# Performance work log

Measured on AMD Instinct MI355X. Metric: run time of the kernel, lower is better.

The kernel has to match this reference:

```python
import jax, jax.numpy as jnp
import numpy as np

BITS = 4
MAXQ = (1 << BITS) - 1      # 15
PACK = 32 // BITS           # 8 values per int32 word
GROUP = 128                 # quantization group size along K


def setup_inputs() -> dict:
    key = jax.random.key(0)
    k0, k1, k2, k3 = jax.random.split(key, 4)
    M, K, N = 4096, 4096, 11008
    G = K // GROUP
    x = jax.random.normal(k0, (M, K), dtype=jnp.float32)
    # packed 4-bit weights: full-range random int32 words (each holds 8 nibbles)
    qweight = jax.random.randint(k1, (K // PACK, N), -(2**31), 2**31 - 1, dtype=jnp.int32)
    # packed zero points: (G, N // PACK) int32 words
    qzeros = jax.random.randint(k2, (G, N // PACK), -(2**31), 2**31 - 1, dtype=jnp.int32)
    # group-wise scales (G, N), small positive values as GPTQ produces
    scales = jax.random.uniform(k3, (G, N), dtype=jnp.float32, minval=1e-3, maxval=1e-2)
    # standard GPTQ grouping: consecutive blocks of GROUP rows share a group
    g_idx = (jnp.arange(K) // GROUP).astype(jnp.int32)
    return {"x": x, "qweight": qweight, "scales": scales, "qzeros": qzeros, "g_idx": g_idx}


def _dequant(qweight, scales, qzeros, g_idx):
    """Unpack int32-packed 4-bit weights and dequantize to float. Returns (K, N)."""
    K = g_idx.shape[0]
    N = qweight.shape[1]
    k = jnp.arange(K)
    # nibble k lives in word k//PACK at bit offset (k%PACK)*BITS
    k_shift = ((k % PACK) * BITS).astype(jnp.int32)
    w = (qweight[k // PACK] >> k_shift[:, None]) & MAXQ              # (K, N) int32 in [0, MAXQ]
    n = jnp.arange(N)
    n_shift = ((n % PACK) * BITS).astype(jnp.int32)
    z = ((qzeros[:, n // PACK] >> n_shift[None, :]) & MAXQ) + 1      # (G, N); kernel adds 1
    return (w - z[g_idx]).astype(scales.dtype) * scales[g_idx]       # (K, N) float


def reference(x, qweight, scales, qzeros, g_idx):
    # C = A @ dequant(B), fp32 accumulation as in the Triton kernel
    W = _dequant(qweight, scales, qzeros, g_idx)
    return jnp.matmul(x, W, preferred_element_type=jnp.float32)
```

## Files before the change

kernel.cpp:

```cpp
#include <hip/hip_runtime.h>
#include <hip/hip_bf16.h>
#include <stdint.h>

typedef _Float16 half8 __attribute__((ext_vector_type(8)));
typedef __attribute__((ext_vector_type(8))) short short8;
typedef __attribute__((ext_vector_type(4))) float floatx4;
typedef __attribute__((ext_vector_type(4))) uint32_t uint32x4;

#define GROUP_SZ 128

__device__ __forceinline__ uint32_t cvt_pk_f16(float lo, float hi) {
    uint32_t r;
    asm("v_cvt_pkrtz_f16_f32 %0, %1, %2" : "=v"(r) : "v"(lo), "v"(hi));
    return r;
}
__device__ __forceinline__ uint32_t pk_add_f16(uint32_t a, uint32_t b) {
    uint32_t r;
    asm("v_pk_add_f16 %0, %1, %2" : "=v"(r) : "v"(a), "v"(b));
    return r;
}
__device__ __forceinline__ uint32_t pk_mul_f16(uint32_t a, uint32_t b) {
    uint32_t r;
    asm("v_pk_mul_f16 %0, %1, %2" : "=v"(r) : "v"(a), "v"(b));
    return r;
}

__global__ __launch_bounds__(256)
void convA_kernel(const float* __restrict__ x, uint4* __restrict__ aws, int total8) {
    int idx = blockIdx.x * 256 + threadIdx.x;
    if (idx >= total8) return;
    const float4* xp = reinterpret_cast<const float4*>(x) + (size_t)idx * 2;
    float4 a = xp[0], b = xp[1];
    uint4 o;
    o.x = cvt_pk_f16(a.x, a.y);
    o.y = cvt_pk_f16(a.z, a.w);
    o.z = cvt_pk_f16(b.x, b.y);
    o.w = cvt_pk_f16(b.z, b.w);
    aws[idx] = o;
}

__global__ __launch_bounds__(256)
void deqB_kernel(const int* __restrict__ qw, const float* __restrict__ sc,
                 const int* __restrict__ qz, char* __restrict__ bws, int K, int N) {
    const int n = blockIdx.x * 256 + threadIdx.x;
    const int wk = blockIdx.y;
    if (n >= N) return;
    const uint32_t w = (uint32_t)qw[(size_t)wk * N + n];
    const int g = wk >> 4;
    const float s = sc[(size_t)g * N + n];
    const uint32_t zw = (uint32_t)qz[(size_t)g * (N >> 3) + (n >> 3)];
    const float zf = -(float)(1025u + ((zw >> ((n & 7) * 4)) & 15u));
    const uint32_t c2 = cvt_pk_f16(zf, zf);
    const uint32_t s2 = cvt_pk_f16(s, s);
    uint32_t oo[4];
    #pragma unroll
    for (int i = 0; i < 4; ++i) {
        const uint32_t tt = w >> (8 * i);
        const uint32_t qi = ((tt & 0xFu) | 0x64006400u) | ((tt << 12) & 0xF0000u);
        oo[i] = pk_mul_f16(pk_add_f16(qi, c2), s2);
    }
    uint4 o; o.x = oo[0]; o.y = oo[1]; o.z = oo[2]; o.w = oo[3];
    const int NKT = K >> 6;
    const int nt = n >> 8, h = (n >> 7) & 1, row = n & 127;
    const int kt = wk >> 3, slot = wk & 7;
    size_t off = ((((size_t)nt * NKT + kt) * 2 + h) * 8 + slot) * 2048 + (size_t)row * 16;
    *reinterpret_cast<uint4*>(bws + off) = o;
}

__global__ __launch_bounds__(512, 2)
void gemm8_kernel(const char* __restrict__ Aws, const char* __restrict__ Bws,
                  float* __restrict__ out, int M, int K, int N) {
    __shared__ char smem[131072];

    const int NT = K >> 6;
    const int nbm = M >> 8, nbn = N >> 8;
    const int nwg = nbm * nbn;
    int bid = blockIdx.x;
    int q = nwg >> 3, r = nwg & 7;
    int xcd = bid & 7, lin = bid >> 3;
    int sid = (xcd < r ? xcd * (q + 1) : r * (q + 1) + (xcd - r) * q) + lin;
    const int bm = sid % nbm, bn = sid / nbm;
    const int m0 = bm << 8, n0 = bn << 8;

    const int tid = threadIdx.x;
    const int lane = tid & 63, w = tid >> 6;
    const int wm = w >> 2, wn = w & 3;
    const int fr = lane & 15, hi = lane >> 4;
    const int r8 = lane >> 3, c8 = lane & 7;

    const uint32_t K2 = (uint32_t)K * 2;
    const char* aBase = Aws + (size_t)m0 * K2;
    uint32_t aOff[2][2];
    #pragma unroll
    for (int h = 0; h < 2; ++h)
        #pragma unroll
        for (int i = 0; i < 2; ++i)
            aOff[h][i] = (uint32_t)(h * 128 + w * 16 + i * 8 + r8) * K2
                       + (uint32_t)((c8 ^ r8) * 16);
    const char* bBase = Bws + (size_t)bn * ((size_t)NT * 32768);
    const uint32_t bOff = (uint32_t)w * 2048u + (uint32_t)lane * 16u;

    auto stageA = [&](uint32_t buf, int h, int kt) {
        #pragma unroll
        for (int i = 0; i < 2; ++i) {
            const char* src = aBase + aOff[h][i] + (uint32_t)kt * 128u;
            char* dst = smem + buf * 65536u + (uint32_t)h * 16384u
                             + (uint32_t)w * 2048u + (uint32_t)i * 1024u;
            __builtin_amdgcn_global_load_lds(
                (const __attribute__((address_space(1))) void*)src,
                (__attribute__((address_space(3))) void*)dst, 16, 0, 0);
        }
    };
    auto stageB = [&](uint32_t buf, int h, int kt) {
        #pragma unroll
        for (int i = 0; i < 2; ++i) {
            const char* src = bBase + bOff + (uint32_t)((kt * 2 + h) * 16384 + i * 1024);
            char* dst = smem + buf * 65536u + 32768u + (uint32_t)h * 16384u
                             + (uint32_t)w * 2048u + (uint32_t)i * 1024u;
            __builtin_amdgcn_global_load_lds(
                (const __attribute__((address_space(1))) void*)src,
                (__attribute__((address_space(3))) void*)dst, 16, 0, 0);
        }
    };

    floatx4 acc[8][4];
    const floatx4 fz = {0.f, 0.f, 0.f, 0.f};
    #pragma unroll
    for (int i = 0; i < 8; ++i)
        #pragma unroll
        for (int j = 0; j < 4; ++j) acc[i][j] = fz;
    half8 af_a[4][2], af_b[4][2];
    half8 bf_x[2][2], bf_y[2][2];

#define LOAD_AF(AF, QM) { _Pragma("unroll") for (int fmi = 0; fmi < 4; ++fmi) { \
    _Pragma("unroll") for (int kk = 0; kk < 2; ++kk) { \
        uint32_t row = (uint32_t)(wm * 128 + ((QM) * 4 + fmi) * 16 + fr); \
        uint32_t p = (uint32_t)((kk * 4 + hi) ^ (fr & 7)); \
        uint32x4 u = *reinterpret_cast<const uint32x4*>(As + row * 128u + p * 16u); \
        AF[fmi][kk] = __builtin_bit_cast(half8, u); } } }

#define LOAD_BF(BF, QN) { _Pragma("unroll") for (int fnj = 0; fnj < 2; ++fnj) { \
    _Pragma("unroll") for (int kk = 0; kk < 2; ++kk) { \
        uint32_t nl = (uint32_t)(wn * 64 + ((QN) * 2 + fnj) * 16 + fr); \
        uint32_t off = (nl >> 7) * 16384u + (uint32_t)(kk * 4 + hi) * 2048u + (nl & 127u) * 16u; \
        uint32x4 u = *reinterpret_cast<const uint32x4*>(Bs + off); \
        BF[fnj][kk] = __builtin_bit_cast(half8, u); } } }

#define MM(AF, BF, QM, QN) { _Pragma("unroll") for (int kk = 0; kk < 2; ++kk) \
    _Pragma("unroll") for (int fmi = 0; fmi < 4; ++fmi) \
    _Pragma("unroll") for (int fnj = 0; fnj < 2; ++fnj) \
        acc[(QM) * 4 + fmi][(QN) * 2 + fnj] = __builtin_amdgcn_mfma_f32_16x16x32_f16( \
            AF[fmi][kk], BF[fnj][kk], acc[(QM) * 4 + fmi][(QN) * 2 + fnj], 0, 0, 0); }

    stageA(0, 0, 0); stageA(0, 1, 0); stageB(0, 0, 0); stageB(0, 1, 0);
    if (NT > 1) { stageA(1, 0, 1); stageA(1, 1, 1); }
    asm volatile("s_waitcnt vmcnt(4)" ::: "memory");
    __builtin_amdgcn_s_barrier();

    for (int t = 0; t < NT; ++t) {
        const uint32_t c = (uint32_t)(t & 1), nb = c ^ 1u;
        const char* As = smem + c * 65536u;
        const char* Bs = As + 32768u;
        const bool st1 = (t + 1 < NT);
        const bool st2 = (t + 2 < NT);
        if (st1) stageB(nb, 0, t + 1);
        LOAD_AF(af_a, 0); LOAD_BF(bf_x, 0);
        __builtin_amdgcn_s_barrier();
        __builtin_amdgcn_s_setprio(1); MM(af_a, bf_x, 0, 0); __builtin_amdgcn_s_setprio(0);
        __builtin_amdgcn_s_barrier();
        if (st1) stageB(nb, 1, t + 1);
        LOAD_AF(af_b, 1);
        __builtin_amdgcn_s_barrier();
        __builtin_amdgcn_s_setprio(1); MM(af_b, bf_x, 1, 0); __builtin_amdgcn_s_setprio(0);
        __builtin_amdgcn_s_barrier();
        if (st2) stageA(c, 0, t + 2);
        LOAD_BF(bf_y, 1);
        __builtin_amdgcn_s_barrier();
        __builtin_amdgcn_s_setprio(1); MM(af_a, bf_y, 0, 1); __builtin_amdgcn_s_setprio(0);
        __builtin_amdgcn_s_barrier();
        if (st2) stageA(c, 1, t + 2);
        __builtin_amdgcn_s_barrier();
        __builtin_amdgcn_s_setprio(1); MM(af_b, bf_y, 1, 1); __builtin_amdgcn_s_setprio(0);
        if (st2) {
            asm volatile("s_waitcnt vmcnt(4)" ::: "memory");
        } else if (st1) {
            asm volatile("s_waitcnt vmcnt(0)" ::: "memory");
        }
        if (st1) __builtin_amdgcn_s_barrier();
    }
#undef LOAD_AF
#undef LOAD_BF
#undef MM

    float* op = out + (size_t)(m0 + wm * 128) * N + n0 + wn * 64;
    #pragma unroll
    for (int fm = 0; fm < 8; ++fm)
        #pragma unroll
        for (int fn = 0; fn < 4; ++fn)
            #pragma unroll
            for (int rr = 0; rr < 4; ++rr)
                op[(size_t)(fm * 16 + hi * 4 + rr) * N + fn * 16 + fr] = acc[fm][fn][rr];
}

__device__ __forceinline__ uint32_t cvt_pk_bf16(float lo, float hi) {
    uint32_t r;
    asm("v_cvt_pk_bf16_f32 %0, %1, %2" : "=v"(r) : "v"(lo), "v"(hi));
    return r;
}
__device__ __forceinline__ uint32_t fswz(uint32_t row, uint32_t byte_in_row) {
    return row * 128u + (byte_in_row ^ ((row & 7u) << 4));
}

__global__ __launch_bounds__(256, 2)
void fused128_kernel(const float* __restrict__ x, const int* __restrict__ qweight,
                     const float* __restrict__ scales, const int* __restrict__ qzeros,
                     float* __restrict__ out, int M, int K, int N) {
    __shared__ char smem[32768];
    char* Ald = smem;
    char* Bld = smem + 16384;
    const int nbm = M / 128, nbn = N / 128;
    const int nwg = nbm * nbn;
    int bid = blockIdx.x;
    int q = nwg >> 3, r = nwg & 7;
    int xcd = bid & 7, lin = bid >> 3;
    int sid = (xcd < r ? xcd * (q + 1) : r * (q + 1) + (xcd - r) * q) + lin;
    int bm = sid / nbn, bn = sid % nbn;
    const int m0 = bm * 128, n0 = bn * 128;
    const int t = threadIdx.x;
    const int lane = t & 63, wave = t >> 6;
    const int tm = t >> 4, tk4 = t & 15;
    const int sn = t & 127, kwh = t >> 7;
    const int gn = n0 + sn;
    const int NT = K / 64;
    float4 av[8]; uint32_t qw[4]; float sc; uint32_t zw;
    const float* xp = x + (size_t)(m0 + tm) * K + tk4 * 4;
    const int* qp = qweight + (size_t)(kwh * 4) * N + gn;
    auto load_tile = [&](int ts) {
        const int k0 = ts * 64;
        #pragma unroll
        for (int i = 0; i < 8; ++i)
            av[i] = *reinterpret_cast<const float4*>(xp + (size_t)i * 16 * K + k0);
        const int g = k0 >> 7;
        sc = scales[(size_t)g * N + gn];
        zw = (uint32_t)qzeros[(size_t)g * (N >> 3) + (gn >> 3)];
        const int* qb = qp + (size_t)(k0 >> 3) * N;
        #pragma unroll
        for (int j = 0; j < 4; ++j) qw[j] = (uint32_t)qb[(size_t)j * N];
    };
    const int zsh = (gn & 7) * 4;
    auto write_tile = [&]() {
        #pragma unroll
        for (int i = 0; i < 8; ++i) {
            uint2 p;
            p.x = cvt_pk_bf16(av[i].x, av[i].y);
            p.y = cvt_pk_bf16(av[i].z, av[i].w);
            *reinterpret_cast<uint2*>(Ald + fswz((uint32_t)(i * 16 + tm), (uint32_t)(tk4 * 8))) = p;
        }
        const float z = (float)((zw >> zsh) & 15u) + 1.0f;
        const float nz = -z * sc;
        #pragma unroll
        for (int j = 0; j < 4; ++j) {
            const uint32_t wv = qw[j];
            float f[8];
            #pragma unroll
            for (int e = 0; e < 8; ++e)
                f[e] = fmaf((float)((wv >> (4 * e)) & 15u), sc, nz);
            uint4 p;
            p.x = cvt_pk_bf16(f[0], f[1]); p.y = cvt_pk_bf16(f[2], f[3]);
            p.z = cvt_pk_bf16(f[4], f[5]); p.w = cvt_pk_bf16(f[6], f[7]);
            *reinterpret_cast<uint4*>(Bld + fswz((uint32_t)sn, (uint32_t)((kwh * 4 + j) * 16))) = p;
        }
    };
    floatx4 acc[4][4];
    const floatx4 fz = {0.f, 0.f, 0.f, 0.f};
    #pragma unroll
    for (int i = 0; i < 4; ++i)
        #pragma unroll
        for (int j = 0; j < 4; ++j) acc[i][j] = fz;
    const int wm = (wave >> 1) * 64, wn = (wave & 1) * 64;
    const int fr = lane & 15;
    const int fkb = ((lane >> 4) * 8) * 2;
    auto compute = [&]() {
        #pragma unroll
        for (int kk = 0; kk < 2; ++kk) {
            short8 afv[4], bfv[4];
            #pragma unroll
            for (int i = 0; i < 4; ++i)
                afv[i] = *reinterpret_cast<const short8*>(
                    Ald + fswz((uint32_t)(wm + i * 16 + fr), (uint32_t)(kk * 64 + fkb)));
            #pragma unroll
            for (int i = 0; i < 4; ++i)
                bfv[i] = *reinterpret_cast<const short8*>(
                    Bld + fswz((uint32_t)(wn + i * 16 + fr), (uint32_t)(kk * 64 + fkb)));
            #pragma unroll
            for (int i = 0; i < 4; ++i)
                #pragma unroll
                for (int j = 0; j < 4; ++j)
                    acc[i][j] = __builtin_amdgcn_mfma_f32_16x16x32_bf16(afv[i], bfv[j], acc[i][j], 0, 0, 0);
        }
    };
    load_tile(0);
    write_tile();
    __syncthreads();
    for (int ts = 0; ts < NT; ++ts) {
        if (ts + 1 < NT) load_tile(ts + 1);
        compute();
        __syncthreads();
        if (ts + 1 < NT) write_tile();
        __syncthreads();
    }
    const int fq = lane >> 4;
    float* op = out + (size_t)(m0 + wm) * N + n0 + wn;
    #pragma unroll
    for (int i = 0; i < 4; ++i)
        #pragma unroll
        for (int j = 0; j < 4; ++j)
            #pragma unroll
            for (int rr = 0; rr < 4; ++rr)
                op[(size_t)(i * 16 + fq * 4 + rr) * N + j * 16 + fr] = acc[i][j][rr];
}

extern "C" void kernel_launch(void* const* d_in, const int* in_sizes, int n_in,
                              void* d_out, int out_size, void* d_ws, size_t ws_size,
                              hipStream_t stream) {
    const float* x       = (const float*)d_in[0];
    const int*   qweight = (const int*)d_in[1];
    const float* scales  = (const float*)d_in[2];
    const int*   qzeros  = (const int*)d_in[3];

    const int K = in_sizes[4];
    const int M = in_sizes[0] / K;
    const int G = K / GROUP_SZ;
    const int N = in_sizes[2] / G;
    float* out = (float*)d_out;

    const size_t needA = (size_t)M * K * 2;
    const size_t needB = (size_t)K * (size_t)N * 2;
    const bool ok = (ws_size >= needA + needB) && (M % 256 == 0) && (N % 256 == 0)
                    && (K % 128 == 0) && (N % 8 == 0);
    if (ok) {
        char* aws = (char*)d_ws;
        char* bws = aws + needA;
        const int total8 = M * (K / 8);
        hipLaunchKernelGGL(convA_kernel, dim3((total8 + 255) / 256), dim3(256), 0, stream,
                           x, (uint4*)aws, total8);
        hipLaunchKernelGGL(deqB_kernel, dim3((N + 255) / 256, K / 8), dim3(256), 0, stream,
                           qweight, scales, qzeros, bws, K, N);
        hipLaunchKernelGGL(gemm8_kernel, dim3((M / 256) * (N / 256)), dim3(512), 0, stream,
                           aws, bws, out, M, K, N);
    } else {
        const int nwg = (M / 128) * (N / 128);
        hipLaunchKernelGGL(fused128_kernel, dim3(nwg), dim3(256), 0, stream,
                           x, qweight, scales, qzeros, out, M, K, N);
    }
}
```

Before: 398.4 us.

## Load B fragments directly from global into registers, drop B LDS staging

B tiles are no longer staged through LDS. Each wave reads its B fragments straight from the pre-swizzled global workspace into registers one K-step ahead, which halves the shared-memory footprint to 64KB. The main loop is restructured to issue all A fragment loads, then MFMA batches interleaved with next-step B global loads, with fewer barriers and adjusted vmcnt waits. The risk is that direct global B loads expose memory latency and duplicate traffic across waves that share the same B columns, and that the register double-buffering may raise register pressure.

```diff
diff --git a/kernel.cpp b/kernel.cpp
--- a/kernel.cpp
+++ b/kernel.cpp
@@ -70,7 +70,7 @@
 __global__ __launch_bounds__(512, 2)
 void gemm8_kernel(const char* __restrict__ Aws, const char* __restrict__ Bws,
                   float* __restrict__ out, int M, int K, int N) {
-    __shared__ char smem[131072];
+    __shared__ char smem[65536];
 
     const int NT = K >> 6;
     const int nbm = M >> 8, nbn = N >> 8;
@@ -98,29 +98,19 @@
             aOff[h][i] = (uint32_t)(h * 128 + w * 16 + i * 8 + r8) * K2
                        + (uint32_t)((c8 ^ r8) * 16);
     const char* bBase = Bws + (size_t)bn * ((size_t)NT * 32768);
-    const uint32_t bOff = (uint32_t)w * 2048u + (uint32_t)lane * 16u;
-
-    auto stageA = [&](uint32_t buf, int h, int kt) {
-        #pragma unroll
-        for (int i = 0; i < 2; ++i) {
-            const char* src = aBase + aOff[h][i] + (uint32_t)kt * 128u;
-            char* dst = smem + buf * 65536u + (uint32_t)h * 16384u
-                             + (uint32_t)w * 2048u + (uint32_t)i * 1024u;
-            __builtin_amdgcn_global_load_lds(
-                (const __attribute__((address_space(1))) void*)src,
-                (__attribute__((address_space(3))) void*)dst, 16, 0, 0);
-        }
-    };
-    auto stageB = [&](uint32_t buf, int h, int kt) {
-        #pragma unroll
-        for (int i = 0; i < 2; ++i) {
-            const char* src = bBase + bOff + (uint32_t)((kt * 2 + h) * 16384 + i * 1024);
-            char* dst = smem + buf * 65536u + 32768u + (uint32_t)h * 16384u
-                             + (uint32_t)w * 2048u + (uint32_t)i * 1024u;
-            __builtin_amdgcn_global_load_lds(
-                (const __attribute__((address_space(1))) void*)src,
-                (__attribute__((address_space(3))) void*)dst, 16, 0, 0);
-        }
+
+    auto stageA = [&](uint32_t buf, int kt) {
+        #pragma unroll
+        for (int h = 0; h < 2; ++h)
+            #pragma unroll
+            for (int i = 0; i < 2; ++i) {
+                const char* src = aBase + aOff[h][i] + (uint32_t)kt * 128u;
+                char* dst = smem + buf * 32768u + (uint32_t)h * 16384u
+                                 + (uint32_t)w * 2048u + (uint32_t)i * 1024u;
+                __builtin_amdgcn_global_load_lds(
+                    (const __attribute__((address_space(1))) void*)src,
+                    (__attribute__((address_space(3))) void*)dst, 16, 0, 0);
+            }
     };
 
     floatx4 acc[8][4];
@@ -139,11 +129,13 @@
         uint32x4 u = *reinterpret_cast<const uint32x4*>(As + row * 128u + p * 16u); \
         AF[fmi][kk] = __builtin_bit_cast(half8, u); } } }
 
-#define LOAD_BF(BF, QN) { _Pragma("unroll") for (int fnj = 0; fnj < 2; ++fnj) { \
+#define LOAD_BFG(BF, QN, KT) { _Pragma("unroll") for (int fnj = 0; fnj < 2; ++fnj) { \
     _Pragma("unroll") for (int kk = 0; kk < 2; ++kk) { \
         uint32_t nl = (uint32_t)(wn * 64 + ((QN) * 2 + fnj) * 16 + fr); \
-        uint32_t off = (nl >> 7) * 16384u + (uint32_t)(kk * 4 + hi) * 2048u + (nl & 127u) * 16u; \
-        uint32x4 u = *reinterpret_cast<const uint32x4*>(Bs + off); \
+        uint32_t slot = (uint32_t)(kk * 4 + hi); \
+        size_t off = ((size_t)((KT) * 2 + (int)(nl >> 7)) * 8 + slot) * 2048 \
+                   + (size_t)(nl & 127u) * 16u; \
+        uint32x4 u = *reinterpret_cast<const uint32x4*>(bBase + off); \
         BF[fnj][kk] = __builtin_bit_cast(half8, u); } } }
 
 #define MM(AF, BF, QM, QN) { _Pragma("unroll") for (int kk = 0; kk < 2; ++kk) \
@@ -152,44 +144,42 @@
         acc[(QM) * 4 + fmi][(QN) * 2 + fnj] = __builtin_amdgcn_mfma_f32_16x16x32_f16( \
             AF[fmi][kk], BF[fnj][kk], acc[(QM) * 4 + fmi][(QN) * 2 + fnj], 0, 0, 0); }
 
-    stageA(0, 0, 0); stageA(0, 1, 0); stageB(0, 0, 0); stageB(0, 1, 0);
-    if (NT > 1) { stageA(1, 0, 1); stageA(1, 1, 1); }
-    asm volatile("s_waitcnt vmcnt(4)" ::: "memory");
+    stageA(0, 0);
+    if (NT > 1) stageA(1, 1);
+    LOAD_BFG(bf_x, 0, 0);
+    LOAD_BFG(bf_y, 1, 0);
+    if (NT > 1) { asm volatile("s_waitcnt vmcnt(12)" ::: "memory"); }
+    else        { asm volatile("s_waitcnt vmcnt(8)" ::: "memory"); }
     __builtin_amdgcn_s_barrier();
 
     for (int t = 0; t < NT; ++t) {
-        const uint32_t c = (uint32_t)(t & 1), nb = c ^ 1u;
-        const char* As = smem + c * 65536u;
-        const char* Bs = As + 32768u;
+        const uint32_t c = (uint32_t)(t & 1);
+        const char* As = smem + c * 32768u;
         const bool st1 = (t + 1 < NT);
         const bool st2 = (t + 2 < NT);
-        if (st1) stageB(nb, 0, t + 1);
-        LOAD_AF(af_a, 0); LOAD_BF(bf_x, 0);
+        LOAD_AF(af_a, 0);
+        LOAD_AF(af_b, 1);
+        __builtin_amdgcn_s_setprio(1);
+        MM(af_a, bf_x, 0, 0);
+        MM(af_b, bf_x, 1, 0);
+        __builtin_amdgcn_s_setprio(0);
+        if (st1) LOAD_BFG(bf_x, 0, t + 1);
+        __builtin_amdgcn_s_setprio(1);
+        MM(af_a, bf_y, 0, 1);
+        MM(af_b, bf_y, 1, 1);
+        __builtin_amdgcn_s_setprio(0);
+        if (st1) LOAD_BFG(bf_y, 1, t + 1);
         __builtin_amdgcn_s_barrier();
-        __builtin_amdgcn_s_setprio(1); MM(af_a, bf_x, 0, 0); __builtin_amdgcn_s_setprio(0);
-        __builtin_amdgcn_s_barrier();
-        if (st1) stageB(nb, 1, t + 1);
-        LOAD_AF(af_b, 1);
-        __builtin_amdgcn_s_barrier();
-        __builtin_amdgcn_s_setprio(1); MM(af_b, bf_x, 1, 0); __builtin_amdgcn_s_setprio(0);
-        __builtin_amdgcn_s_barrier();
-        if (st2) stageA(c, 0, t + 2);
-        LOAD_BF(bf_y, 1);
-        __builtin_amdgcn_s_barrier();
-        __builtin_amdgcn_s_setprio(1); MM(af_a, bf_y, 0, 1); __builtin_amdgcn_s_setprio(0);
-        __builtin_amdgcn_s_barrier();
-        if (st2) stageA(c, 1, t + 2);
-        __builtin_amdgcn_s_barrier();
-        __builtin_amdgcn_s_setprio(1); MM(af_b, bf_y, 1, 1); __builtin_amdgcn_s_setprio(0);
         if (st2) {
-            asm volatile("s_waitcnt vmcnt(4)" ::: "memory");
+            stageA(c, t + 2);
+            asm volatile("s_waitcnt vmcnt(12)" ::: "memory");
         } else if (st1) {
-            asm volatile("s_waitcnt vmcnt(0)" ::: "memory");
+            asm volatile("s_waitcnt vmcnt(8)" ::: "memory");
         }
         if (st1) __builtin_amdgcn_s_barrier();
     }
 #undef LOAD_AF
-#undef LOAD_BF
+#undef LOAD_BFG
 #undef MM
 
     float* op = out + (size_t)(m0 + wm * 128) * N + n0 + wn * 64;
```

After: 388.0 us. -2.6%, faster.
